# Kernel tuning notes

Hardware: AMD Instinct MI355X
Metric: run time of the kernel (lower is better)

## Reference

```python
import jax, jax.numpy as jnp
import numpy as np

DEPTH, HEADS, DIM_HEAD, DIM = 4, 8, 64, 512
B, N = 4, 512
SCALE = DIM_HEAD ** -0.5  # attention scale
EPS = 1e-5


def _ln(r, g, b):
    # naive real-valued LayerNorm over last dim
    m = jnp.mean(r, -1, keepdims=True)
    v = jnp.mean((r - m) ** 2, -1, keepdims=True)
    return (r - m) / jnp.sqrt(v + EPS) * g + b


def _cln(z, gr, br, gi, bi):
    # 'layer_norm_naive': LN applied separately to real and imag parts
    return jax.lax.complex(_ln(jnp.real(z), gr, br), _ln(jnp.imag(z), gi, bi))


def _csoftmax(z):
    # softmax on magnitude, phase preserved (Eq. 36, arXiv:1802.08026)
    p = jax.nn.softmax(jnp.abs(z), axis=-1)
    ph = jnp.angle(z)
    return jax.lax.complex(p * jnp.cos(ph), p * jnp.sin(ph))


def _crelu(z):
    return jax.lax.complex(jax.nn.relu(jnp.real(z)), jax.nn.relu(jnp.imag(z)))


def setup_inputs():
    key = jax.random.key(0)
    ks = jax.random.split(key, 8)
    s = np.float32(1.0 / np.sqrt(DIM))
    return dict(
        x_real=jax.random.normal(ks[0], (B, N, DIM), jnp.float32),
        x_imag=jax.random.normal(ks[1], (B, N, DIM), jnp.float32),
        ln1_g_r=jnp.ones((DEPTH, DIM), jnp.float32),
        ln1_b_r=jnp.zeros((DEPTH, DIM), jnp.float32),
        ln1_g_i=jnp.ones((DEPTH, DIM), jnp.float32),
        ln1_b_i=jnp.zeros((DEPTH, DIM), jnp.float32),
        ln2_g_r=jnp.ones((DEPTH, DIM), jnp.float32),
        ln2_b_r=jnp.zeros((DEPTH, DIM), jnp.float32),
        ln2_g_i=jnp.ones((DEPTH, DIM), jnp.float32),
        ln2_b_i=jnp.zeros((DEPTH, DIM), jnp.float32),
        qkv_w_r=jax.random.normal(ks[2], (DEPTH, DIM, DIM), jnp.float32) * s,
        qkv_w_i=jax.random.normal(ks[3], (DEPTH, DIM, DIM), jnp.float32) * s,
        out_w_r=jax.random.normal(ks[4], (DEPTH, DIM, DIM), jnp.float32) * s,
        out_w_i=jax.random.normal(ks[5], (DEPTH, DIM, DIM), jnp.float32) * s,
        out_b_r=jnp.zeros((DEPTH, DIM), jnp.float32),
        out_b_i=jnp.zeros((DEPTH, DIM), jnp.float32),
        ff_w_r=jax.random.normal(ks[6], (DEPTH, DIM, DIM), jnp.float32) * s,
        ff_w_i=jax.random.normal(ks[7], (DEPTH, DIM, DIM), jnp.float32) * s,
        step_size=jnp.full((DEPTH,), 0.1, jnp.float32),
        lambd=jnp.full((DEPTH,), 0.1, jnp.float32),
    )


def reference(x_real, x_imag,
              ln1_g_r, ln1_b_r, ln1_g_i, ln1_b_i,
              ln2_g_r, ln2_b_r, ln2_g_i, ln2_b_i,
              qkv_w_r, qkv_w_i, out_w_r, out_w_i, out_b_r, out_b_i,
              ff_w_r, ff_w_i, step_size, lambd):
    x = jax.lax.complex(x_real, x_imag)  # [B, N, DIM] complex64
    for l in range(DEPTH):
        Wqkv = jax.lax.complex(qkv_w_r[l], qkv_w_i[l])  # [inner, dim]
        Wout = jax.lax.complex(out_w_r[l], out_w_i[l])  # [dim, inner]
        bout = jax.lax.complex(out_b_r[l], out_b_i[l])
        Wff = jax.lax.complex(ff_w_r[l], ff_w_i[l])     # [dim, dim]
        # --- PreNorm + Attention (single shared QKV projection) + residual
        xn = _cln(x, ln1_g_r[l], ln1_b_r[l], ln1_g_i[l], ln1_b_i[l])
        w = jnp.einsum('bnd,ed->bne', xn, Wqkv)                 # complex linear, no bias
        w = w.reshape(B, N, HEADS, DIM_HEAD).transpose(0, 2, 1, 3)  # b h n d
        dots = jnp.einsum('bhnd,bhmd->bhnm', w, jnp.conj(w)) * SCALE
        attn = _csoftmax(dots)
        out = jnp.einsum('bhnm,bhmd->bhnd', attn, w)
        out = out.transpose(0, 2, 1, 3).reshape(B, N, HEADS * DIM_HEAD)
        out = jnp.einsum('bne,de->bnd', out, Wout) + bout
        x = out + x
        # --- PreNorm + ISTA-style FeedForward (CReLU); no outer residual
        xn = _cln(x, ln2_g_r[l], ln2_b_r[l], ln2_g_i[l], ln2_b_i[l])
        ss = jax.nn.softplus(step_size[l])
        lm = jax.nn.softplus(lambd[l])
        x1 = jnp.einsum('bnd,ed->bne', xn, Wff)
        x = _crelu(xn + ss * x1 - ss * lm)
    # stack real/imag so the output is a plain float tensor [2, B, N, DIM]
    return jnp.stack([jnp.real(x), jnp.imag(x)], axis=0)
```

## Files before the change

### kernel.cpp

```cpp
#include <hip/hip_runtime.h>
#include <math.h>

#define DEPTHL 4
#define HEADS 8
#define DH 64
#define DIM 512
#define BATCH 4
#define SEQ 512
#define ROWS (BATCH*SEQ)
#define SCALE 0.125f
#define LNEPS 1e-5f

typedef __attribute__((ext_vector_type(8))) short bfrag;
typedef __attribute__((ext_vector_type(4))) float ffrag;
#define MFMA(a,b,c) __builtin_amdgcn_mfma_f32_16x16x32_bf16(a, b, c, 0, 0, 0)

__device__ __forceinline__ unsigned short f2bf(float f) {
    unsigned int u = __float_as_uint(f);
    u += 0x7fffu + ((u >> 16) & 1u);
    return (unsigned short)(u >> 16);
}
__device__ __forceinline__ float bf2f(unsigned short b) {
    return __uint_as_float(((unsigned int)b) << 16);
}

__global__ __launch_bounds__(256) void convw(
    const float* __restrict__ s0, const float* __restrict__ s1,
    const float* __restrict__ s2, const float* __restrict__ s3,
    const float* __restrict__ s4, const float* __restrict__ s5,
    unsigned short* __restrict__ dst)
{
    int gid = blockIdx.x * 256 + threadIdx.x;
    int idx = gid * 4;
    int seg = idx >> 18;
    int off = idx & 262143;
    const float* s = seg == 0 ? s0 : seg == 1 ? s1 : seg == 2 ? s2 :
                     seg == 3 ? s3 : seg == 4 ? s4 : s5;
    float4 v = *(const float4*)(s + off);
    unsigned long long p = (unsigned long long)f2bf(v.x)
        | ((unsigned long long)f2bf(v.y) << 16)
        | ((unsigned long long)f2bf(v.z) << 32)
        | ((unsigned long long)f2bf(v.w) << 48);
    *(unsigned long long*)(dst + idx) = p;
}

__device__ __forceinline__ void blk_sum4(float& a, float& b, float& c, float& d) {
    __shared__ float s[16];
    #pragma unroll
    for (int o = 32; o; o >>= 1) {
        a += __shfl_xor(a, o); b += __shfl_xor(b, o);
        c += __shfl_xor(c, o); d += __shfl_xor(d, o);
    }
    int w = threadIdx.x >> 6;
    if ((threadIdx.x & 63) == 0) { s[w*4+0]=a; s[w*4+1]=b; s[w*4+2]=c; s[w*4+3]=d; }
    __syncthreads();
    a = s[0]+s[4]+s[8]+s[12];
    b = s[1]+s[5]+s[9]+s[13];
    c = s[2]+s[6]+s[10]+s[14];
    d = s[3]+s[7]+s[11]+s[15];
    __syncthreads();
}

__global__ __launch_bounds__(256) void ln_kernel(
    const float* __restrict__ xr, const float* __restrict__ xi,
    const float* __restrict__ gr, const float* __restrict__ br,
    const float* __restrict__ gi, const float* __restrict__ bi,
    unsigned short* __restrict__ outr, unsigned short* __restrict__ outi)
{
    int row = blockIdx.x, t = threadIdx.x;
    float2 vr = ((const float2*)(xr + (size_t)row*DIM))[t];
    float2 vi = ((const float2*)(xi + (size_t)row*DIM))[t];
    float sr = vr.x+vr.y, qr = vr.x*vr.x+vr.y*vr.y;
    float si = vi.x+vi.y, qi = vi.x*vi.x+vi.y*vi.y;
    blk_sum4(sr, qr, si, qi);
    float mr = sr*(1.f/DIM), mi_ = si*(1.f/DIM);
    float rr = 1.f/sqrtf(qr*(1.f/DIM)-mr*mr+LNEPS);
    float ri = 1.f/sqrtf(qi*(1.f/DIM)-mi_*mi_+LNEPS);
    float2 g2r = ((const float2*)gr)[t], b2r = ((const float2*)br)[t];
    float2 g2i = ((const float2*)gi)[t], b2i = ((const float2*)bi)[t];
    float o0 = (vr.x-mr)*rr*g2r.x + b2r.x;
    float o1 = (vr.y-mr)*rr*g2r.y + b2r.y;
    float o2 = (vi.x-mi_)*ri*g2i.x + b2i.x;
    float o3 = (vi.y-mi_)*ri*g2i.y + b2i.y;
    unsigned int pr = (unsigned int)f2bf(o0) | ((unsigned int)f2bf(o1) << 16);
    unsigned int pi = (unsigned int)f2bf(o2) | ((unsigned int)f2bf(o3) << 16);
    ((unsigned int*)(outr + (size_t)row*DIM))[t] = pr;
    ((unsigned int*)(outi + (size_t)row*DIM))[t] = pi;
}

template<int MODE>
__global__ __launch_bounds__(256, 4) void cgemm_mfma(
    const unsigned short* __restrict__ Ar, const unsigned short* __restrict__ Ai,
    const unsigned short* __restrict__ Wr, const unsigned short* __restrict__ Wi,
    unsigned short* __restrict__ Obr, unsigned short* __restrict__ Obi,
    float* __restrict__ Ofr, float* __restrict__ Ofi,
    const float* __restrict__ biasR, const float* __restrict__ biasI,
    const float* __restrict__ stepp, const float* __restrict__ lamb, int layer)
{
    int tid = threadIdx.x;
    int lane = tid & 63;
    int w = tid >> 6, wr = w >> 1, wc = w & 1;
    int lrow = lane & 15, lg = lane >> 4;
    int bm = blockIdx.x, bn = blockIdx.y;

    const unsigned short* pAr = Ar + (size_t)(bm*32 + wr*16 + lrow)*DIM + lg*8;
    const unsigned short* pAi = Ai + (size_t)(bm*32 + wr*16 + lrow)*DIM + lg*8;
    const unsigned short* pBr[2]; const unsigned short* pBi[2];
    #pragma unroll
    for (int nt = 0; nt < 2; ++nt) {
        int brow = bn*64 + wc*32 + nt*16 + lrow;
        pBr[nt] = Wr + (size_t)brow*DIM + lg*8;
        pBi[nt] = Wi + (size_t)brow*DIM + lg*8;
    }
    ffrag acc1[2], acc2[2], acci[2];
    #pragma unroll
    for (int nt = 0; nt < 2; ++nt) {
        acc1[nt] = (ffrag){0.f,0.f,0.f,0.f};
        acc2[nt] = (ffrag){0.f,0.f,0.f,0.f};
        acci[nt] = (ffrag){0.f,0.f,0.f,0.f};
    }

    bfrag a_r = *(const bfrag*)(pAr);
    bfrag a_i = *(const bfrag*)(pAi);
    bfrag b_r0 = *(const bfrag*)(pBr[0]), b_r1 = *(const bfrag*)(pBr[1]);
    bfrag b_i0 = *(const bfrag*)(pBi[0]), b_i1 = *(const bfrag*)(pBi[1]);

    #pragma unroll 2
    for (int k0 = 0; k0 < DIM - 32; k0 += 32) {
        bfrag na_r = *(const bfrag*)(pAr + k0 + 32);
        bfrag na_i = *(const bfrag*)(pAi + k0 + 32);
        bfrag nb_r0 = *(const bfrag*)(pBr[0] + k0 + 32);
        bfrag nb_r1 = *(const bfrag*)(pBr[1] + k0 + 32);
        bfrag nb_i0 = *(const bfrag*)(pBi[0] + k0 + 32);
        bfrag nb_i1 = *(const bfrag*)(pBi[1] + k0 + 32);
        acc1[0] = MFMA(a_r, b_r0, acc1[0]);
        acc2[0] = MFMA(a_i, b_i0, acc2[0]);
        acci[0] = MFMA(a_r, b_i0, acci[0]);
        acci[0] = MFMA(a_i, b_r0, acci[0]);
        acc1[1] = MFMA(a_r, b_r1, acc1[1]);
        acc2[1] = MFMA(a_i, b_i1, acc2[1]);
        acci[1] = MFMA(a_r, b_i1, acci[1]);
        acci[1] = MFMA(a_i, b_r1, acci[1]);
        a_r = na_r; a_i = na_i;
        b_r0 = nb_r0; b_r1 = nb_r1; b_i0 = nb_i0; b_i1 = nb_i1;
    }
    acc1[0] = MFMA(a_r, b_r0, acc1[0]);
    acc2[0] = MFMA(a_i, b_i0, acc2[0]);
    acci[0] = MFMA(a_r, b_i0, acci[0]);
    acci[0] = MFMA(a_i, b_r0, acci[0]);
    acc1[1] = MFMA(a_r, b_r1, acc1[1]);
    acc2[1] = MFMA(a_i, b_i1, acc2[1]);
    acci[1] = MFMA(a_r, b_i1, acci[1]);
    acci[1] = MFMA(a_i, b_r1, acci[1]);

    float ss = 0.f, sl = 0.f;
    if (MODE == 2) { ss = log1pf(expf(stepp[layer])); sl = ss * log1pf(expf(lamb[layer])); }

    #pragma unroll
    for (int nt = 0; nt < 2; ++nt) {
        int E = bn*64 + wc*32 + nt*16 + lrow;
        #pragma unroll
        for (int r = 0; r < 4; ++r) {
            int R = bm*32 + wr*16 + lg*4 + r;
            float re = acc1[nt][r] - acc2[nt][r];
            float im = acci[nt][r];
            if (MODE == 0) {
                int b = R >> 9, n = R & (SEQ-1);
                int h = E >> 6, d = E & 63;
                size_t off = (((size_t)(b*HEADS + h)*SEQ + n) << 6) + d;
                Obr[off] = f2bf(re);
                Obi[off] = f2bf(im);
            } else if (MODE == 1) {
                size_t off = (size_t)R*DIM + E;
                Ofr[off] = re + biasR[E] + Ofr[off];
                Ofi[off] = im + biasI[E] + Ofi[off];
            } else {
                size_t off = (size_t)R*DIM + E;
                float xnr_ = bf2f(Ar[off]), xni_ = bf2f(Ai[off]);
                Ofr[off] = fmaxf(xnr_ + ss*re - sl, 0.f);
                Ofi[off] = fmaxf(xni_ + ss*im, 0.f);
            }
        }
    }
}

#define SVI(w_, ri, d, m) ((((w_)*2 + (ri))*64 + (d))*40 + (m))
#define SPI(w_, ri, q, m) (20480 + (((w_)*2 + (ri))*16 + (q))*40 + (m))

__global__ __launch_bounds__(256, 3) void attn_mfma(
    const unsigned short* __restrict__ whr, const unsigned short* __restrict__ whi,
    unsigned short* __restrict__ aor, unsigned short* __restrict__ aoi)
{
    __shared__ __align__(16) unsigned short pool[25856];
    float* sMS = (float*)(pool + 25600);
    float* sAccR = (float*)pool;
    float* sAccI = sAccR + 64*16;

    int tid = threadIdx.x, lane = tid & 63, w = tid >> 6;
    int lrow = lane & 15, lg = lane >> 4;
    int bh = blockIdx.x, qt = blockIdx.y;
    const unsigned short* baseR = whr + ((size_t)bh << 15);
    const unsigned short* baseI = whi + ((size_t)bh << 15);
    int q0 = qt*16;

    bfrag qfr[2], qfi[2];
    #pragma unroll
    for (int ks = 0; ks < 2; ++ks) {
        qfr[ks] = *(const bfrag*)(baseR + ((size_t)(q0 + lrow) << 6) + ks*32 + lg*8);
        qfi[ks] = *(const bfrag*)(baseI + ((size_t)(q0 + lrow) << 6) + ks*32 + lg*8);
    }
    float M = -1e30f, S = 0.f;
    ffrag o1[4], o2[4], o3[4];
    #pragma unroll
    for (int dt = 0; dt < 4; ++dt) {
        o1[dt] = (ffrag){0.f,0.f,0.f,0.f};
        o2[dt] = (ffrag){0.f,0.f,0.f,0.f};
        o3[dt] = (ffrag){0.f,0.f,0.f,0.f};
    }
    const int sm = lane & 31;
    const int sdb = ((lane >> 5) & 1) * 8;

    #pragma unroll 1
    for (int rd = 0; rd < 4; ++rd) {
        int m0 = rd*128 + w*32;
        #pragma unroll
        for (int it = 0; it < 4; ++it) {
            int d0 = sdb + it*16;
            bfrag vr = *(const bfrag*)(baseR + ((size_t)(m0 + sm) << 6) + d0);
            bfrag vi = *(const bfrag*)(baseI + ((size_t)(m0 + sm) << 6) + d0);
            #pragma unroll
            for (int j = 0; j < 8; ++j) {
                pool[SVI(w, 0, d0 + j, sm)] = (unsigned short)vr[j];
                pool[SVI(w, 1, d0 + j, sm)] = (unsigned short)vi[j];
            }
        }
        ffrag zr[2], zp[2], zm_[2];
        #pragma unroll
        for (int t = 0; t < 2; ++t) {
            zr[t] = (ffrag){0.f,0.f,0.f,0.f};
            zp[t] = (ffrag){0.f,0.f,0.f,0.f};
            zm_[t] = (ffrag){0.f,0.f,0.f,0.f};
        }
        #pragma unroll
        for (int t = 0; t < 2; ++t)
        #pragma unroll
        for (int ks = 0; ks < 2; ++ks) {
            bfrag kr = *(const bfrag*)(baseR + ((size_t)(m0 + t*16 + lrow) << 6) + ks*32 + lg*8);
            bfrag ki = *(const bfrag*)(baseI + ((size_t)(m0 + t*16 + lrow) << 6) + ks*32 + lg*8);
            zr[t]  = MFMA(kr, qfr[ks], zr[t]);
            zr[t]  = MFMA(ki, qfi[ks], zr[t]);
            zp[t]  = MFMA(kr, qfi[ks], zp[t]);
            zm_[t] = MFMA(ki, qfr[ks], zm_[t]);
        }
        float av[2][4], rv[2][4], iv[2][4];
        float pmax = -1e30f;
        #pragma unroll
        for (int t = 0; t < 2; ++t)
        #pragma unroll
        for (int r = 0; r < 4; ++r) {
            float zrv = zr[t][r] * SCALE;
            float ziv = (zp[t][r] - zm_[t][r]) * SCALE;
            float a = sqrtf(zrv*zrv + ziv*ziv);
            av[t][r] = a; rv[t][r] = zrv; iv[t][r] = ziv;
            pmax = fmaxf(pmax, a);
        }
        pmax = fmaxf(pmax, __shfl_xor(pmax, 16));
        pmax = fmaxf(pmax, __shfl_xor(pmax, 32));
        float Mnew = fmaxf(M, pmax);
        float f = expf(M - Mnew);
        M = Mnew;
        S *= f;
        #pragma unroll
        for (int dt = 0; dt < 4; ++dt) { o1[dt] *= f; o2[dt] *= f; o3[dt] *= f; }
        float ssum = 0.f;
        #pragma unroll
        for (int t = 0; t < 2; ++t) {
            float ur[4], ui[4];
            #pragma unroll
            for (int r = 0; r < 4; ++r) {
                float a = av[t][r];
                float ee = expf(a - M);
                ssum += ee;
                float inva = a > 0.f ? ee / a : 0.f;
                ur[r] = a > 0.f ? inva * rv[t][r] : ee;
                ui[r] = inva * iv[t][r];
            }
            uint2 wpr, wpi;
            wpr.x = (unsigned int)f2bf(ur[0]) | ((unsigned int)f2bf(ur[1]) << 16);
            wpr.y = (unsigned int)f2bf(ur[2]) | ((unsigned int)f2bf(ur[3]) << 16);
            wpi.x = (unsigned int)f2bf(ui[0]) | ((unsigned int)f2bf(ui[1]) << 16);
            wpi.y = (unsigned int)f2bf(ui[2]) | ((unsigned int)f2bf(ui[3]) << 16);
            *(uint2*)&pool[SPI(w, 0, lrow, t*16 + lg*4)] = wpr;
            *(uint2*)&pool[SPI(w, 1, lrow, t*16 + lg*4)] = wpi;
        }
        ssum += __shfl_xor(ssum, 16);
        ssum += __shfl_xor(ssum, 32);
        S += ssum;
        bfrag pr = *(const bfrag*)&pool[SPI(w, 0, lrow, lg*8)];
        bfrag pi = *(const bfrag*)&pool[SPI(w, 1, lrow, lg*8)];
        #pragma unroll
        for (int dt = 0; dt < 4; ++dt) {
            bfrag vr = *(const bfrag*)&pool[SVI(w, 0, dt*16 + lrow, lg*8)];
            bfrag vi = *(const bfrag*)&pool[SVI(w, 1, dt*16 + lrow, lg*8)];
            o1[dt] = MFMA(vr, pr, o1[dt]);
            o2[dt] = MFMA(vi, pi, o2[dt]);
            o3[dt] = MFMA(vr, pi, o3[dt]);
            o3[dt] = MFMA(vi, pr, o3[dt]);
        }
    }

    if (lg == 0) { sMS[(w*2 + 0)*16 + lrow] = M; sMS[(w*2 + 1)*16 + lrow] = S; }
    __syncthreads();
    float Mf = -1e30f;
    #pragma unroll
    for (int w2 = 0; w2 < 4; ++w2) Mf = fmaxf(Mf, sMS[(w2*2 + 0)*16 + lrow]);
    float Sf = 0.f;
    #pragma unroll
    for (int w2 = 0; w2 < 4; ++w2)
        Sf += sMS[(w2*2 + 1)*16 + lrow] * expf(sMS[(w2*2 + 0)*16 + lrow] - Mf);
    float fac = expf(M - Mf) / Sf;

    #pragma unroll 1
    for (int ww = 0; ww < 4; ++ww) {
        if (w == ww) {
            #pragma unroll
            for (int dt = 0; dt < 4; ++dt)
            #pragma unroll
            for (int r = 0; r < 4; ++r) {
                int d = dt*16 + lg*4 + r;
                float vR = (o1[dt][r] - o2[dt][r]) * fac;
                float vI = o3[dt][r] * fac;
                if (ww == 0) { sAccR[d*16 + lrow] = vR; sAccI[d*16 + lrow] = vI; }
                else         { sAccR[d*16 + lrow] += vR; sAccI[d*16 + lrow] += vI; }
            }
        }
        __syncthreads();
    }
    {
        int q = tid >> 4, d0 = (tid & 15) * 4;
        int b = bh >> 3, h = bh & 7;
        float r0 = sAccR[(d0+0)*16 + q], r1 = sAccR[(d0+1)*16 + q];
        float r2 = sAccR[(d0+2)*16 + q], r3 = sAccR[(d0+3)*16 + q];
        float i0 = sAccI[(d0+0)*16 + q], i1 = sAccI[(d0+1)*16 + q];
        float i2 = sAccI[(d0+2)*16 + q], i3 = sAccI[(d0+3)*16 + q];
        uint2 pr, pi;
        pr.x = (unsigned int)f2bf(r0) | ((unsigned int)f2bf(r1) << 16);
        pr.y = (unsigned int)f2bf(r2) | ((unsigned int)f2bf(r3) << 16);
        pi.x = (unsigned int)f2bf(i0) | ((unsigned int)f2bf(i1) << 16);
        pi.y = (unsigned int)f2bf(i2) | ((unsigned int)f2bf(i3) << 16);
        size_t off = (((size_t)(bh >> 3)*SEQ + qt*16 + q) << 9) + (bh & 7)*64 + d0;
        *(uint2*)(aor + off) = pr;
        *(uint2*)(aoi + off) = pi;
    }
}

extern "C" void kernel_launch(void* const* d_in, const int* in_sizes, int n_in,
                              void* d_out, int out_size, void* d_ws, size_t ws_size,
                              hipStream_t stream)
{
    const float* x_real  = (const float*)d_in[0];
    const float* x_imag  = (const float*)d_in[1];
    const float* ln1_g_r = (const float*)d_in[2];
    const float* ln1_b_r = (const float*)d_in[3];
    const float* ln1_g_i = (const float*)d_in[4];
    const float* ln1_b_i = (const float*)d_in[5];
    const float* ln2_g_r = (const float*)d_in[6];
    const float* ln2_b_r = (const float*)d_in[7];
    const float* ln2_g_i = (const float*)d_in[8];
    const float* ln2_b_i = (const float*)d_in[9];
    const float* qkv_w_r = (const float*)d_in[10];
    const float* qkv_w_i = (const float*)d_in[11];
    const float* out_w_r = (const float*)d_in[12];
    const float* out_w_i = (const float*)d_in[13];
    const float* out_b_r = (const float*)d_in[14];
    const float* out_b_i = (const float*)d_in[15];
    const float* ff_w_r  = (const float*)d_in[16];
    const float* ff_w_i  = (const float*)d_in[17];
    const float* stepp   = (const float*)d_in[18];
    const float* lamb    = (const float*)d_in[19];

    const size_t SZ = (size_t)ROWS * DIM;
    const size_t WSEG = (size_t)DIM * DIM;
    float* xr = (float*)d_ws;
    float* xi = xr + SZ;
    unsigned short* xnr = (unsigned short*)(xi + SZ);
    unsigned short* xni = xnr + SZ;
    unsigned short* whr = xni + SZ;
    unsigned short* whi = whr + SZ;
    unsigned short* aor = whi + SZ;
    unsigned short* aoi = aor + SZ;
    unsigned short* wb  = aoi + SZ;

    float* outR = (float*)d_out;
    float* outI = outR + SZ;

    hipMemcpyAsync(xr, x_real, SZ*sizeof(float), hipMemcpyDeviceToDevice, stream);
    hipMemcpyAsync(xi, x_imag, SZ*sizeof(float), hipMemcpyDeviceToDevice, stream);

    for (int l = 0; l < DEPTHL; ++l) {
        const size_t WO = (size_t)l * WSEG;
        convw<<<1536, 256, 0, stream>>>(qkv_w_r + WO, qkv_w_i + WO, out_w_r + WO,
                                        out_w_i + WO, ff_w_r + WO, ff_w_i + WO, wb);
        ln_kernel<<<ROWS, 256, 0, stream>>>(xr, xi,
            ln1_g_r + l*DIM, ln1_b_r + l*DIM, ln1_g_i + l*DIM, ln1_b_i + l*DIM, xnr, xni);
        cgemm_mfma<0><<<dim3(64, 8), 256, 0, stream>>>(xnr, xni, wb, wb + WSEG,
            whr, whi, nullptr, nullptr, nullptr, nullptr, nullptr, nullptr, l);
        attn_mfma<<<dim3(32, 32), 256, 0, stream>>>(whr, whi, aor, aoi);
        cgemm_mfma<1><<<dim3(64, 8), 256, 0, stream>>>(aor, aoi, wb + 2*WSEG, wb + 3*WSEG,
            nullptr, nullptr, xr, xi, out_b_r + l*DIM, out_b_i + l*DIM, nullptr, nullptr, l);
        ln_kernel<<<ROWS, 256, 0, stream>>>(xr, xi,
            ln2_g_r + l*DIM, ln2_b_r + l*DIM, ln2_g_i + l*DIM, ln2_b_i + l*DIM, xnr, xni);
        float* dstR = (l == DEPTHL-1) ? outR : xr;
        float* dstI = (l == DEPTHL-1) ? outI : xi;
        cgemm_mfma<2><<<dim3(64, 8), 256, 0, stream>>>(xnr, xni, wb + 4*WSEG, wb + 5*WSEG,
            nullptr, nullptr, dstR, dstI, nullptr, nullptr, stepp, lamb, l);
    }
}
```

Baseline: 657.8 us.

## Split fused flash attention into QK, softmax, PV kernels with materialized scores

Replaces the single online-softmax attention kernel with four kernels. One transposes V, one writes fp16 QK scores to a global buffer, one does the complex magnitude softmax in place and stores bf16 probabilities, and one runs an MFMA PV GEMM. The goal is to drop the per-tile rescaling, the LDS transpose of V and the serialized cross-warp reduction of the old kernel, giving more parallel blocks in exchange for large score-matrix traffic (32 heads × 512×512 × 2 parts). Weight bf16 conversion is also hoisted out of the layer loop into one launch covering all layers.

```diff
diff --git a/kernel.cpp b/kernel.cpp
--- a/kernel.cpp
+++ b/kernel.cpp
@@ -13,6 +13,9 @@
 
 typedef __attribute__((ext_vector_type(8))) short bfrag;
 typedef __attribute__((ext_vector_type(4))) float ffrag;
+typedef __attribute__((ext_vector_type(2))) _Float16 h2;
+typedef __attribute__((ext_vector_type(4))) unsigned short u16x4;
+typedef __attribute__((ext_vector_type(8))) unsigned short u16x8;
 #define MFMA(a,b,c) __builtin_amdgcn_mfma_f32_16x16x32_bf16(a, b, c, 0, 0, 0)
 
 __device__ __forceinline__ unsigned short f2bf(float f) {
@@ -30,10 +33,9 @@
     const float* __restrict__ s4, const float* __restrict__ s5,
     unsigned short* __restrict__ dst)
 {
-    int gid = blockIdx.x * 256 + threadIdx.x;
-    int idx = gid * 4;
-    int seg = idx >> 18;
-    int off = idx & 262143;
+    size_t idx = ((size_t)blockIdx.x * 256 + threadIdx.x) * 4;
+    int seg = (int)(idx >> 20);
+    int off = (int)(idx & 1048575);
     const float* s = seg == 0 ? s0 : seg == 1 ? s1 : seg == 2 ? s2 :
                      seg == 3 ? s3 : seg == 4 ? s4 : s5;
     float4 v = *(const float4*)(s + off);
@@ -184,173 +186,195 @@
     }
 }
 
-#define SVI(w_, ri, d, m) ((((w_)*2 + (ri))*64 + (d))*40 + (m))
-#define SPI(w_, ri, q, m) (20480 + (((w_)*2 + (ri))*16 + (q))*40 + (m))
-
-__global__ __launch_bounds__(256, 3) void attn_mfma(
+__global__ __launch_bounds__(256) void vT_kernel(
     const unsigned short* __restrict__ whr, const unsigned short* __restrict__ whi,
-    unsigned short* __restrict__ aor, unsigned short* __restrict__ aoi)
-{
-    __shared__ __align__(16) unsigned short pool[25856];
-    float* sMS = (float*)(pool + 25600);
-    float* sAccR = (float*)pool;
-    float* sAccI = sAccR + 64*16;
-
-    int tid = threadIdx.x, lane = tid & 63, w = tid >> 6;
+    unsigned short* __restrict__ whTr, unsigned short* __restrict__ whTi)
+{
+    __shared__ unsigned short sR[64][68], sI[64][68];
+    int tid = threadIdx.x, mt = blockIdx.x, bh = blockIdx.y;
+    const unsigned short* bR = whr + ((size_t)bh << 15) + (size_t)(mt << 6) * 64;
+    const unsigned short* bI = whi + ((size_t)bh << 15) + (size_t)(mt << 6) * 64;
+    int ml = tid >> 4, d4 = (tid & 15) * 4;
+    #pragma unroll
+    for (int jj = 0; jj < 4; ++jj) {
+        int r_ = ml + jj*16;
+        *(u16x4*)&sR[r_][d4] = *(const u16x4*)(bR + r_*64 + d4);
+        *(u16x4*)&sI[r_][d4] = *(const u16x4*)(bI + r_*64 + d4);
+    }
+    __syncthreads();
+    int d = tid >> 2, mo = (tid & 3) * 16;
+    u16x8 vr0, vr1, vi0, vi1;
+    #pragma unroll
+    for (int jj = 0; jj < 8; ++jj) {
+        vr0[jj] = sR[mo + jj][d];      vr1[jj] = sR[mo + 8 + jj][d];
+        vi0[jj] = sI[mo + jj][d];      vi1[jj] = sI[mo + 8 + jj][d];
+    }
+    size_t off = ((size_t)bh*64 + d)*512 + (mt << 6) + mo;
+    *(u16x8*)(whTr + off) = vr0;  *(u16x8*)(whTr + off + 8) = vr1;
+    *(u16x8*)(whTi + off) = vi0;  *(u16x8*)(whTi + off + 8) = vi1;
+}
+
+__global__ __launch_bounds__(256) void qk_kernel(
+    const unsigned short* __restrict__ whr, const unsigned short* __restrict__ whi,
+    _Float16* __restrict__ Zr, _Float16* __restrict__ Zi)
+{
+    int tid = threadIdx.x, lane = tid & 63;
+    int w = tid >> 6, wr = w >> 1, wc = w & 1;
     int lrow = lane & 15, lg = lane >> 4;
-    int bh = blockIdx.x, qt = blockIdx.y;
+    int qt = blockIdx.x, mt = blockIdx.y, bh = blockIdx.z;
     const unsigned short* baseR = whr + ((size_t)bh << 15);
     const unsigned short* baseI = whi + ((size_t)bh << 15);
-    int q0 = qt*16;
-
-    bfrag qfr[2], qfi[2];
-    #pragma unroll
-    for (int ks = 0; ks < 2; ++ks) {
-        qfr[ks] = *(const bfrag*)(baseR + ((size_t)(q0 + lrow) << 6) + ks*32 + lg*8);
-        qfi[ks] = *(const bfrag*)(baseI + ((size_t)(q0 + lrow) << 6) + ks*32 + lg*8);
-    }
-    float M = -1e30f, S = 0.f;
-    ffrag o1[4], o2[4], o3[4];
-    #pragma unroll
-    for (int dt = 0; dt < 4; ++dt) {
-        o1[dt] = (ffrag){0.f,0.f,0.f,0.f};
-        o2[dt] = (ffrag){0.f,0.f,0.f,0.f};
-        o3[dt] = (ffrag){0.f,0.f,0.f,0.f};
-    }
-    const int sm = lane & 31;
-    const int sdb = ((lane >> 5) & 1) * 8;
-
-    #pragma unroll 1
-    for (int rd = 0; rd < 4; ++rd) {
-        int m0 = rd*128 + w*32;
-        #pragma unroll
-        for (int it = 0; it < 4; ++it) {
-            int d0 = sdb + it*16;
-            bfrag vr = *(const bfrag*)(baseR + ((size_t)(m0 + sm) << 6) + d0);
-            bfrag vi = *(const bfrag*)(baseI + ((size_t)(m0 + sm) << 6) + d0);
-            #pragma unroll
-            for (int j = 0; j < 8; ++j) {
-                pool[SVI(w, 0, d0 + j, sm)] = (unsigned short)vr[j];
-                pool[SVI(w, 1, d0 + j, sm)] = (unsigned short)vi[j];
-            }
-        }
-        ffrag zr[2], zp[2], zm_[2];
-        #pragma unroll
-        for (int t = 0; t < 2; ++t) {
-            zr[t] = (ffrag){0.f,0.f,0.f,0.f};
-            zp[t] = (ffrag){0.f,0.f,0.f,0.f};
-            zm_[t] = (ffrag){0.f,0.f,0.f,0.f};
-        }
-        #pragma unroll
-        for (int t = 0; t < 2; ++t)
-        #pragma unroll
-        for (int ks = 0; ks < 2; ++ks) {
-            bfrag kr = *(const bfrag*)(baseR + ((size_t)(m0 + t*16 + lrow) << 6) + ks*32 + lg*8);
-            bfrag ki = *(const bfrag*)(baseI + ((size_t)(m0 + t*16 + lrow) << 6) + ks*32 + lg*8);
-            zr[t]  = MFMA(kr, qfr[ks], zr[t]);
-            zr[t]  = MFMA(ki, qfi[ks], zr[t]);
-            zp[t]  = MFMA(kr, qfi[ks], zp[t]);
-            zm_[t] = MFMA(ki, qfr[ks], zm_[t]);
-        }
-        float av[2][4], rv[2][4], iv[2][4];
-        float pmax = -1e30f;
-        #pragma unroll
-        for (int t = 0; t < 2; ++t)
+    int qrow = qt*32 + wr*16 + lrow;
+    bfrag qr0 = *(const bfrag*)(baseR + (qrow << 6) + lg*8);
+    bfrag qr1 = *(const bfrag*)(baseR + (qrow << 6) + 32 + lg*8);
+    bfrag qi0 = *(const bfrag*)(baseI + (qrow << 6) + lg*8);
+    bfrag qi1 = *(const bfrag*)(baseI + (qrow << 6) + 32 + lg*8);
+
+    ffrag aRR[2], aII[2], aIR[2], aRI[2];
+    #pragma unroll
+    for (int nt = 0; nt < 2; ++nt) {
+        aRR[nt] = (ffrag){0.f,0.f,0.f,0.f};
+        aII[nt] = (ffrag){0.f,0.f,0.f,0.f};
+        aIR[nt] = (ffrag){0.f,0.f,0.f,0.f};
+        aRI[nt] = (ffrag){0.f,0.f,0.f,0.f};
+    }
+    #pragma unroll
+    for (int nt = 0; nt < 2; ++nt) {
+        int mrow = mt*64 + wc*32 + nt*16 + lrow;
+        bfrag kr0 = *(const bfrag*)(baseR + (mrow << 6) + lg*8);
+        bfrag kr1 = *(const bfrag*)(baseR + (mrow << 6) + 32 + lg*8);
+        bfrag ki0 = *(const bfrag*)(baseI + (mrow << 6) + lg*8);
+        bfrag ki1 = *(const bfrag*)(baseI + (mrow << 6) + 32 + lg*8);
+        aRR[nt] = MFMA(qr0, kr0, aRR[nt]);  aRR[nt] = MFMA(qr1, kr1, aRR[nt]);
+        aII[nt] = MFMA(qi0, ki0, aII[nt]);  aII[nt] = MFMA(qi1, ki1, aII[nt]);
+        aIR[nt] = MFMA(qi0, kr0, aIR[nt]);  aIR[nt] = MFMA(qi1, kr1, aIR[nt]);
+        aRI[nt] = MFMA(qr0, ki0, aRI[nt]);  aRI[nt] = MFMA(qr1, ki1, aRI[nt]);
+    }
+    #pragma unroll
+    for (int nt = 0; nt < 2; ++nt) {
+        int m = mt*64 + wc*32 + nt*16 + lrow;
         #pragma unroll
         for (int r = 0; r < 4; ++r) {
-            float zrv = zr[t][r] * SCALE;
-            float ziv = (zp[t][r] - zm_[t][r]) * SCALE;
-            float a = sqrtf(zrv*zrv + ziv*ziv);
-            av[t][r] = a; rv[t][r] = zrv; iv[t][r] = ziv;
-            pmax = fmaxf(pmax, a);
+            int q = qt*32 + wr*16 + lg*4 + r;
+            size_t off = ((size_t)bh << 18) + ((size_t)q << 9) + m;
+            Zr[off] = (_Float16)((aRR[nt][r] + aII[nt][r]) * SCALE);
+            Zi[off] = (_Float16)((aIR[nt][r] - aRI[nt][r]) * SCALE);
         }
-        pmax = fmaxf(pmax, __shfl_xor(pmax, 16));
-        pmax = fmaxf(pmax, __shfl_xor(pmax, 32));
-        float Mnew = fmaxf(M, pmax);
-        float f = expf(M - Mnew);
-        M = Mnew;
-        S *= f;
+    }
+}
+
+__global__ __launch_bounds__(256) void sm_kernel(
+    _Float16* __restrict__ Zr, _Float16* __restrict__ Zi)
+{
+    int tid = threadIdx.x, lane = tid & 63, w = tid >> 6;
+    size_t row = (size_t)blockIdx.x * 4 + w;
+    _Float16* pr = Zr + (row << 9);
+    _Float16* pi = Zi + (row << 9);
+    float zr[8], zi[8], av[8], ev[8];
+    float mx = -1e30f;
+    #pragma unroll
+    for (int j = 0; j < 4; ++j) {
+        int m = j*128 + lane*2;
+        h2 vr = *(const h2*)(pr + m);
+        h2 vi = *(const h2*)(pi + m);
+        zr[2*j] = (float)vr[0]; zr[2*j+1] = (float)vr[1];
+        zi[2*j] = (float)vi[0]; zi[2*j+1] = (float)vi[1];
+    }
+    #pragma unroll
+    for (int j = 0; j < 8; ++j) {
+        av[j] = sqrtf(zr[j]*zr[j] + zi[j]*zi[j]);
+        mx = fmaxf(mx, av[j]);
+    }
+    #pragma unroll
+    for (int o = 32; o; o >>= 1) mx = fmaxf(mx, __shfl_xor(mx, o));
+    float s = 0.f;
+    #pragma unroll
+    for (int j = 0; j < 8; ++j) { ev[j] = expf(av[j] - mx); s += ev[j]; }
+    #pragma unroll
+    for (int o = 32; o; o >>= 1) s += __shfl_xor(s, o);
+    float inv = 1.f / s;
+    #pragma unroll
+    for (int j = 0; j < 4; ++j) {
+        int m = j*128 + lane*2;
+        float p0 = ev[2*j] * inv,  p1 = ev[2*j+1] * inv;
+        float f0 = av[2*j]   > 0.f ? p0 / av[2*j]   : 0.f;
+        float f1 = av[2*j+1] > 0.f ? p1 / av[2*j+1] : 0.f;
+        float or0 = av[2*j]   > 0.f ? f0*zr[2*j]   : p0;
+        float or1 = av[2*j+1] > 0.f ? f1*zr[2*j+1] : p1;
+        float oi0 = f0*zi[2*j], oi1 = f1*zi[2*j+1];
+        *(unsigned int*)(pr + m) = (unsigned int)f2bf(or0) | ((unsigned int)f2bf(or1) << 16);
+        *(unsigned int*)(pi + m) = (unsigned int)f2bf(oi0) | ((unsigned int)f2bf(oi1) << 16);
+    }
+}
+
+__global__ __launch_bounds__(256, 4) void pv_kernel(
+    const unsigned short* __restrict__ Pr, const unsigned short* __restrict__ Pi,
+    const unsigned short* __restrict__ whTr, const unsigned short* __restrict__ whTi,
+    unsigned short* __restrict__ aor, unsigned short* __restrict__ aoi)
+{
+    int tid = threadIdx.x, lane = tid & 63;
+    int w = tid >> 6, wr = w >> 1, wc = w & 1;
+    int lrow = lane & 15, lg = lane >> 4;
+    int qt = blockIdx.x, bh = blockIdx.y;
+
+    const unsigned short* pA_r = Pr + ((size_t)bh << 18) + ((size_t)(qt*32 + wr*16 + lrow) << 9) + lg*8;
+    const unsigned short* pA_i = Pi + ((size_t)bh << 18) + ((size_t)(qt*32 + wr*16 + lrow) << 9) + lg*8;
+    const unsigned short* pB_r0 = whTr + ((size_t)bh*64 + wc*32 + lrow)*512 + lg*8;
+    const unsigned short* pB_i0 = whTi + ((size_t)bh*64 + wc*32 + lrow)*512 + lg*8;
+    const unsigned short* pB_r1 = pB_r0 + (size_t)16*512;
+    const unsigned short* pB_i1 = pB_i0 + (size_t)16*512;
+
+    ffrag c1[2], c2[2], ci[2];
+    #pragma unroll
+    for (int nt = 0; nt < 2; ++nt) {
+        c1[nt] = (ffrag){0.f,0.f,0.f,0.f};
+        c2[nt] = (ffrag){0.f,0.f,0.f,0.f};
+        ci[nt] = (ffrag){0.f,0.f,0.f,0.f};
+    }
+    bfrag a_r = *(const bfrag*)(pA_r);
+    bfrag a_i = *(const bfrag*)(pA_i);
+    bfrag b_r0 = *(const bfrag*)(pB_r0), b_r1 = *(const bfrag*)(pB_r1);
+    bfrag b_i0 = *(const bfrag*)(pB_i0), b_i1 = *(const bfrag*)(pB_i1);
+
+    #pragma unroll 2
+    for (int k0 = 0; k0 < 512 - 32; k0 += 32) {
+        bfrag na_r  = *(const bfrag*)(pA_r  + k0 + 32);
+        bfrag na_i  = *(const bfrag*)(pA_i  + k0 + 32);
+        bfrag nb_r0 = *(const bfrag*)(pB_r0 + k0 + 32);
+        bfrag nb_r1 = *(const bfrag*)(pB_r1 + k0 + 32);
+        bfrag nb_i0 = *(const bfrag*)(pB_i0 + k0 + 32);
+        bfrag nb_i1 = *(const bfrag*)(pB_i1 + k0 + 32);
+        c1[0] = MFMA(a_r, b_r0, c1[0]);
+        c2[0] = MFMA(a_i, b_i0, c2[0]);
+        ci[0] = MFMA(a_r, b_i0, ci[0]);
+        ci[0] = MFMA(a_i, b_r0, ci[0]);
+        c1[1] = MFMA(a_r, b_r1, c1[1]);
+        c2[1] = MFMA(a_i, b_i1, c2[1]);
+        ci[1] = MFMA(a_r, b_i1, ci[1]);
+        ci[1] = MFMA(a_i, b_r1, ci[1]);
+        a_r = na_r; a_i = na_i;
+        b_r0 = nb_r0; b_r1 = nb_r1; b_i0 = nb_i0; b_i1 = nb_i1;
+    }
+    c1[0] = MFMA(a_r, b_r0, c1[0]);
+    c2[0] = MFMA(a_i, b_i0, c2[0]);
+    ci[0] = MFMA(a_r, b_i0, ci[0]);
+    ci[0] = MFMA(a_i, b_r0, ci[0]);
+    c1[1] = MFMA(a_r, b_r1, c1[1]);
+    c2[1] = MFMA(a_i, b_i1, c2[1]);
+    ci[1] = MFMA(a_r, b_i1, ci[1]);
+    ci[1] = MFMA(a_i, b_r1, ci[1]);
+
+    int b = bh >> 3, h = bh & 7;
+    #pragma unroll
+    for (int nt = 0; nt < 2; ++nt) {
+        int d = wc*32 + nt*16 + lrow;
         #pragma unroll
-        for (int dt = 0; dt < 4; ++dt) { o1[dt] *= f; o2[dt] *= f; o3[dt] *= f; }
-        float ssum = 0.f;
-        #pragma unroll
-        for (int t = 0; t < 2; ++t) {
-            float ur[4], ui[4];
-            #pragma unroll
-            for (int r = 0; r < 4; ++r) {
-                float a = av[t][r];
-                float ee = expf(a - M);
-                ssum += ee;
-                float inva = a > 0.f ? ee / a : 0.f;
-                ur[r] = a > 0.f ? inva * rv[t][r] : ee;
-                ui[r] = inva * iv[t][r];
-            }
-            uint2 wpr, wpi;
-            wpr.x = (unsigned int)f2bf(ur[0]) | ((unsigned int)f2bf(ur[1]) << 16);
-            wpr.y = (unsigned int)f2bf(ur[2]) | ((unsigned int)f2bf(ur[3]) << 16);
-            wpi.x = (unsigned int)f2bf(ui[0]) | ((unsigned int)f2bf(ui[1]) << 16);
-            wpi.y = (unsigned int)f2bf(ui[2]) | ((unsigned int)f2bf(ui[3]) << 16);
-            *(uint2*)&pool[SPI(w, 0, lrow, t*16 + lg*4)] = wpr;
-            *(uint2*)&pool[SPI(w, 1, lrow, t*16 + lg*4)] = wpi;
+        for (int r = 0; r < 4; ++r) {
+            int q = qt*32 + wr*16 + lg*4 + r;
+            size_t off = (((size_t)(b*SEQ + q)) << 9) + h*64 + d;
+            aor[off] = f2bf(c1[nt][r] - c2[nt][r]);
+            aoi[off] = f2bf(ci[nt][r]);
         }
-        ssum += __shfl_xor(ssum, 16);
-        ssum += __shfl_xor(ssum, 32);
-        S += ssum;
-        bfrag pr = *(const bfrag*)&pool[SPI(w, 0, lrow, lg*8)];
-        bfrag pi = *(const bfrag*)&pool[SPI(w, 1, lrow, lg*8)];
-        #pragma unroll
-        for (int dt = 0; dt < 4; ++dt) {
-            bfrag vr = *(const bfrag*)&pool[SVI(w, 0, dt*16 + lrow, lg*8)];
-            bfrag vi = *(const bfrag*)&pool[SVI(w, 1, dt*16 + lrow, lg*8)];
-            o1[dt] = MFMA(vr, pr, o1[dt]);
-            o2[dt] = MFMA(vi, pi, o2[dt]);
-            o3[dt] = MFMA(vr, pi, o3[dt]);
-            o3[dt] = MFMA(vi, pr, o3[dt]);
-        }
-    }
-
-    if (lg == 0) { sMS[(w*2 + 0)*16 + lrow] = M; sMS[(w*2 + 1)*16 + lrow] = S; }
-    __syncthreads();
-    float Mf = -1e30f;
-    #pragma unroll
-    for (int w2 = 0; w2 < 4; ++w2) Mf = fmaxf(Mf, sMS[(w2*2 + 0)*16 + lrow]);
-    float Sf = 0.f;
-    #pragma unroll
-    for (int w2 = 0; w2 < 4; ++w2)
-        Sf += sMS[(w2*2 + 1)*16 + lrow] * expf(sMS[(w2*2 + 0)*16 + lrow] - Mf);
-    float fac = expf(M - Mf) / Sf;
-
-    #pragma unroll 1
-    for (int ww = 0; ww < 4; ++ww) {
-        if (w == ww) {
-            #pragma unroll
-            for (int dt = 0; dt < 4; ++dt)
-            #pragma unroll
-            for (int r = 0; r < 4; ++r) {
-                int d = dt*16 + lg*4 + r;
-                float vR = (o1[dt][r] - o2[dt][r]) * fac;
-                float vI = o3[dt][r] * fac;
-                if (ww == 0) { sAccR[d*16 + lrow] = vR; sAccI[d*16 + lrow] = vI; }
-                else         { sAccR[d*16 + lrow] += vR; sAccI[d*16 + lrow] += vI; }
-            }
-        }
-        __syncthreads();
-    }
-    {
-        int q = tid >> 4, d0 = (tid & 15) * 4;
-        int b = bh >> 3, h = bh & 7;
-        float r0 = sAccR[(d0+0)*16 + q], r1 = sAccR[(d0+1)*16 + q];
-        float r2 = sAccR[(d0+2)*16 + q], r3 = sAccR[(d0+3)*16 + q];
-        float i0 = sAccI[(d0+0)*16 + q], i1 = sAccI[(d0+1)*16 + q];
-        float i2 = sAccI[(d0+2)*16 + q], i3 = sAccI[(d0+3)*16 + q];
-        uint2 pr, pi;
-        pr.x = (unsigned int)f2bf(r0) | ((unsigned int)f2bf(r1) << 16);
-        pr.y = (unsigned int)f2bf(r2) | ((unsigned int)f2bf(r3) << 16);
-        pi.x = (unsigned int)f2bf(i0) | ((unsigned int)f2bf(i1) << 16);
-        pi.y = (unsigned int)f2bf(i2) | ((unsigned int)f2bf(i3) << 16);
-        size_t off = (((size_t)(bh >> 3)*SEQ + qt*16 + q) << 9) + (bh & 7)*64 + d0;
-        *(uint2*)(aor + off) = pr;
-        *(uint2*)(aoi + off) = pi;
     }
 }
 
@@ -381,15 +405,20 @@
 
     const size_t SZ = (size_t)ROWS * DIM;
     const size_t WSEG = (size_t)DIM * DIM;
+    const size_t WALL = 4 * WSEG;
     float* xr = (float*)d_ws;
     float* xi = xr + SZ;
-    unsigned short* xnr = (unsigned short*)(xi + SZ);
-    unsigned short* xni = xnr + SZ;
-    unsigned short* whr = xni + SZ;
-    unsigned short* whi = whr + SZ;
-    unsigned short* aor = whi + SZ;
-    unsigned short* aoi = aor + SZ;
-    unsigned short* wb  = aoi + SZ;
+    unsigned short* xnr  = (unsigned short*)(xi + SZ);
+    unsigned short* xni  = xnr + SZ;
+    unsigned short* whr  = xni + SZ;
+    unsigned short* whi  = whr + SZ;
+    unsigned short* aor  = whi + SZ;
+    unsigned short* aoi  = aor + SZ;
+    unsigned short* whTr = aoi + SZ;
+    unsigned short* whTi = whTr + SZ;
+    unsigned short* wb   = whTi + SZ;
+    _Float16* Zr = (_Float16*)(wb + 6*WALL);
+    _Float16* Zi = Zr + ((size_t)32 << 18);
 
     float* outR = (float*)d_out;
     float* outI = outR + SZ;
@@ -397,22 +426,33 @@
     hipMemcpyAsync(xr, x_real, SZ*sizeof(float), hipMemcpyDeviceToDevice, stream);
     hipMemcpyAsync(xi, x_imag, SZ*sizeof(float), hipMemcpyDeviceToDevice, stream);
 
+    convw<<<6144, 256, 0, stream>>>(qkv_w_r, qkv_w_i, out_w_r, out_w_i, ff_w_r, ff_w_i, wb);
+
     for (int l = 0; l < DEPTHL; ++l) {
         const size_t WO = (size_t)l * WSEG;
-        convw<<<1536, 256, 0, stream>>>(qkv_w_r + WO, qkv_w_i + WO, out_w_r + WO,
-                                        out_w_i + WO, ff_w_r + WO, ff_w_i + WO, wb);
+        const unsigned short* Wq_r = wb + 0*WALL + WO;
+        const unsigned short* Wq_i = wb + 1*WALL + WO;
+        const unsigned short* Wo_r = wb + 2*WALL + WO;
+        const unsigned short* Wo_i = wb + 3*WALL + WO;
+        const unsigned short* Wf_r = wb + 4*WALL + WO;
+        const unsigned short* Wf_i = wb + 5*WALL + WO;
+
         ln_kernel<<<ROWS, 256, 0, stream>>>(xr, xi,
             ln1_g_r + l*DIM, ln1_b_r + l*DIM, ln1_g_i + l*DIM, ln1_b_i + l*DIM, xnr, xni);
-        cgemm_mfma<0><<<dim3(64, 8), 256, 0, stream>>>(xnr, xni, wb, wb + WSEG,
+        cgemm_mfma<0><<<dim3(64, 8), 256, 0, stream>>>(xnr, xni, Wq_r, Wq_i,
             whr, whi, nullptr, nullptr, nullptr, nullptr, nullptr, nullptr, l);
-        attn_mfma<<<dim3(32, 32), 256, 0, stream>>>(whr, whi, aor, aoi);
-        cgemm_mfma<1><<<dim3(64, 8), 256, 0, stream>>>(aor, aoi, wb + 2*WSEG, wb + 3*WSEG,
+        vT_kernel<<<dim3(8, 32), 256, 0, stream>>>(whr, whi, whTr, whTi);
+        qk_kernel<<<dim3(16, 8, 32), 256, 0, stream>>>(whr, whi, Zr, Zi);
+        sm_kernel<<<4096, 256, 0, stream>>>(Zr, Zi);
+        pv_kernel<<<dim3(16, 32), 256, 0, stream>>>(
+            (const unsigned short*)Zr, (const unsigned short*)Zi, whTr, whTi, aor, aoi);
+        cgemm_mfma<1><<<dim3(64, 8), 256, 0, stream>>>(aor, aoi, Wo_r, Wo_i,
             nullptr, nullptr, xr, xi, out_b_r + l*DIM, out_b_i + l*DIM, nullptr, nullptr, l);
         ln_kernel<<<ROWS, 256, 0, stream>>>(xr, xi,
             ln2_g_r + l*DIM, ln2_b_r + l*DIM, ln2_g_i + l*DIM, ln2_b_i + l*DIM, xnr, xni);
         float* dstR = (l == DEPTHL-1) ? outR : xr;
         float* dstI = (l == DEPTHL-1) ? outI : xi;
-        cgemm_mfma<2><<<dim3(64, 8), 256, 0, stream>>>(xnr, xni, wb + 4*WSEG, wb + 5*WSEG,
+        cgemm_mfma<2><<<dim3(64, 8), 256, 0, stream>>>(xnr, xni, Wf_r, Wf_i,
             nullptr, nullptr, dstR, dstI, nullptr, nullptr, stepp, lamb, l);
     }
 }
```

After: 746.2 us. 13.4% more time.
